# Performance work log

Measured on AMD Instinct MI355X. Metric: run time of the kernel, lower is better.

The kernel has to match this reference:

```python
import jax, jax.numpy as jnp
import numpy as np

B, T, D, H = 8, 2048, 1024, 64

def setup_inputs() -> dict:
    key = jax.random.key(0)
    ks = jax.random.split(key, 4)
    s = 1.0 / np.sqrt(D)
    return {
        "x": jax.random.normal(ks[0], (B, T, D), dtype=jnp.float32),
        "Wk": jax.random.normal(ks[1], (D, H), dtype=jnp.float32) * s,
        "bk": jnp.zeros((H,), dtype=jnp.float32),
        "Wq": jax.random.normal(ks[2], (D, H), dtype=jnp.float32) * s,
        "bq": jnp.zeros((H,), dtype=jnp.float32),
        "Wv": jax.random.normal(ks[3], (D, H), dtype=jnp.float32) * s,
        "bv": jnp.zeros((H,), dtype=jnp.float32),
    }

def reference(x, Wk, bk, Wq, bq, Wv, bv):
    # Linear projections: [B, T, H]
    k = x @ Wk + bk
    q = x @ Wq + bq
    v = x @ Wv + bv
    hs = k.shape[-1]
    # Scaled scores [B, T, T]
    scores = jnp.einsum('bqh,bkh->bqk', q, k) * (1.0 / np.sqrt(hs))
    # Causal mask (tril): positions j > i get -inf
    t = x.shape[1]
    causal = jnp.tril(jnp.ones((t, t), dtype=bool))
    scores = jnp.where(causal, scores, -jnp.inf)
    attn = jax.nn.softmax(scores, axis=-1)
    # Dropout is identity in eval mode
    return jnp.einsum('bqk,bkh->bqh', attn, v)
```

## Files before the change

kernel.cpp:

```cpp
#include <hip/hip_runtime.h>
#include <hip/hip_bf16.h>
#include <cmath>

#define B_ 8
#define T_ 2048
#define D_ 1024
#define H_ 64

typedef __bf16 bf16x8 __attribute__((ext_vector_type(8)));
typedef __bf16 bf16x4 __attribute__((ext_vector_type(4)));
typedef float f32x4 __attribute__((ext_vector_type(4)));

#define QSCALE 0.18033688011112042f

__device__ __forceinline__ void async_copy16(const void* g, void* lds) {
  __builtin_amdgcn_global_load_lds(
      (const __attribute__((address_space(1))) unsigned int*)g,
      (__attribute__((address_space(3))) unsigned int*)lds,
      16, 0, 0);
}

__global__ __launch_bounds__(256)
void castw_kernel(const float* __restrict__ w0,
                  const float* __restrict__ w1,
                  const float* __restrict__ w2,
                  __bf16* __restrict__ Wt) {
  __shared__ float tile[64][65];
  const int mat = blockIdx.y;
  const float* w = (mat == 0) ? w0 : (mat == 1) ? w1 : w2;
  const int d0 = blockIdx.x * 64;
  const int t = threadIdx.x;
#pragma unroll
  for (int i = 0; i < 16; i++) {
    int idx = i * 256 + t;
    int dl = idx >> 6, h = idx & 63;
    tile[dl][h] = w[(size_t)(d0 + dl) * 64 + h];
  }
  __syncthreads();
  const int h = t >> 2;
  const int dc = (t & 3) * 16;
  bf16x8 o0, o1;
#pragma unroll
  for (int j = 0; j < 8; j++) {
    o0[j] = (__bf16)tile[dc + j][h];
    o1[j] = (__bf16)tile[dc + 8 + j][h];
  }
  bf16x8* dst = (bf16x8*)(Wt + (size_t)mat * 65536 + (size_t)h * 1024 + d0 + dc);
  dst[0] = o0;
  dst[1] = o1;
}

__global__ __launch_bounds__(256)
void proj_kernel(const float* __restrict__ x,
                 const __bf16* __restrict__ Wt,
                 const float* __restrict__ bq,
                 const float* __restrict__ bk,
                 const float* __restrict__ bv,
                 __bf16* __restrict__ qb,
                 __bf16* __restrict__ kb,
                 __bf16* __restrict__ vt) {
  __shared__ __align__(16) __bf16 xs[32 * 128];
  __shared__ __align__(16) __bf16 wsl[192 * 128];

  const int tid  = threadIdx.x;
  const int wv   = tid >> 6;
  const int lane = tid & 63;
  const int ln   = lane & 15;
  const int quad = lane >> 4;
  const int m0   = blockIdx.x * 32;

  f32x4 acc[6] = {};

  for (int s = 0; s < 8; s++) {
    const int k0 = s * 128;
    __syncthreads();

#pragma unroll
    for (int j = 0; j < 12; j++) {
      int i = wv * 12 + j;
      int grow = i * 4 + (lane >> 4);
      int kc = (lane & 15) ^ (grow & 15);
      const __bf16* gp = Wt + (size_t)grow * 1024 + k0 + kc * 8;
      async_copy16(gp, wsl + i * 512);
    }

#pragma unroll
    for (int u = 0; u < 2; u++)
#pragma unroll
      for (int kh = 0; kh < 2; kh++) {
        int row = (tid >> 4) + u * 16;
        int fi = (tid & 15) + kh * 16;
        float4 f = *(const float4*)(x + (size_t)(m0 + row) * D_ + k0 + fi * 4);
        bf16x4 hv;
        hv[0] = (__bf16)f.x; hv[1] = (__bf16)f.y;
        hv[2] = (__bf16)f.z; hv[3] = (__bf16)f.w;
        int ch = fi >> 1, half = fi & 1;
        *(bf16x4*)(xs + row * 128 + ((ch ^ (row & 15)) * 8) + half * 4) = hv;
      }

    __syncthreads();

#pragma unroll
    for (int ks = 0; ks < 4; ks++) {
      bf16x8 af[2];
#pragma unroll
      for (int mt = 0; mt < 2; mt++) {
        int m = mt * 16 + ln;
        af[mt] = *(const bf16x8*)(xs + m * 128 + (((ks * 4 + quad) ^ (m & 15)) * 8));
      }
#pragma unroll
      for (int nt = 0; nt < 3; nt++) {
        int col = wv * 48 + nt * 16 + ln;
        bf16x8 bf = *(const bf16x8*)(wsl + col * 128 + (((ks * 4 + quad) ^ (col & 15)) * 8));
#pragma unroll
        for (int mt = 0; mt < 2; mt++)
          acc[mt * 3 + nt] =
              __builtin_amdgcn_mfma_f32_16x16x32_bf16(af[mt], bf, acc[mt * 3 + nt], 0, 0, 0);
      }
    }
  }

#pragma unroll
  for (int nt = 0; nt < 3; nt++) {
    int idx = wv * 48 + nt * 16;
    int mat = idx >> 6;
    int h = (idx & 63) + ln;
    float bcol = ((mat == 0) ? bq : (mat == 1) ? bk : bv)[h];
#pragma unroll
    for (int mt = 0; mt < 2; mt++) {
      f32x4 a = acc[mt * 3 + nt];
      int grow0 = m0 + mt * 16 + quad * 4;
      if (mat == 0) {
#pragma unroll
        for (int r = 0; r < 4; r++)
          qb[(size_t)(grow0 + r) * 64 + h] = (__bf16)((a[r] + bcol) * QSCALE);
      } else if (mat == 1) {
#pragma unroll
        for (int r = 0; r < 4; r++)
          kb[(size_t)(grow0 + r) * 64 + h] = (__bf16)(a[r] + bcol);
      } else {
        int bb = grow0 >> 11, t0 = grow0 & 2047;
        bf16x4 pv;
#pragma unroll
        for (int r = 0; r < 4; r++)
          pv[r] = (__bf16)(a[r] + bcol);
        *(bf16x4*)(vt + (size_t)(bb * 64 + h) * T_ + t0) = pv;
      }
    }
  }
}

__global__ __launch_bounds__(256)
void attn_kernel(const __bf16* __restrict__ qb,
                 const __bf16* __restrict__ kb,
                 const __bf16* __restrict__ vt,
                 float* __restrict__ out) {
  __shared__ __align__(16) __bf16 pA[2][4][16][72];
  __shared__ float ml_m[4][16];
  __shared__ float ml_l[4][16];
  __shared__ float olds[4][16][64];

  const int tid   = threadIdx.x;
  const int wv    = tid >> 6;
  const int lane  = tid & 63;
  const int ln    = lane & 15;
  const int quad  = lane >> 4;
  const int b     = blockIdx.y;

  const int p     = ((blockIdx.y >> 2) & 1) ? blockIdx.x : 63 - blockIdx.x;
  const int jqL   = p, jqH = 127 - p;
  const int qbL   = jqL * 16, qbH = jqH * 16;
  const int ntL   = (jqL >> 2) + 1;
  const int ntH   = (jqH >> 2) + 1;

  const __bf16* Q = qb + (size_t)b * T_ * 64;
  const __bf16* K = kb + (size_t)b * T_ * 64;
  const __bf16* V = vt + (size_t)b * 64 * T_;

  bf16x8 qaL0 = *(const bf16x8*)(Q + (qbL + ln) * 64 + quad * 8);
  bf16x8 qaL1 = *(const bf16x8*)(Q + (qbL + ln) * 64 + 32 + quad * 8);
  bf16x8 qaH0 = *(const bf16x8*)(Q + (qbH + ln) * 64 + quad * 8);
  bf16x8 qaH1 = *(const bf16x8*)(Q + (qbH + ln) * 64 + 32 + quad * 8);

  f32x4 accL[4] = {}, accH[4] = {};
  float mL = -INFINITY, lL = 0.f, mH = -INFINITY, lH = 0.f;

  bf16x8 kfa[4], kfb[4], vfa[4], vfb[4];
#pragma unroll
  for (int h = 0; h < 4; h++) {
    const __bf16* kr = K + (size_t)(wv * 64 + h * 16 + ln) * 64 + quad * 8;
    kfa[h] = *(const bf16x8*)kr;
    kfb[h] = *(const bf16x8*)(kr + 32);
  }

  int jt = wv;

  for (; jt < ntL; jt += 4) {
    const int kv0 = jt * 64;

    f32x4 sH[4] = {}, sL[4] = {};
#pragma unroll
    for (int h = 0; h < 4; h++) {
      sH[h] = __builtin_amdgcn_mfma_f32_16x16x32_bf16(kfa[h], qaH0, sH[h], 0, 0, 0);
      sH[h] = __builtin_amdgcn_mfma_f32_16x16x32_bf16(kfb[h], qaH1, sH[h], 0, 0, 0);
      sL[h] = __builtin_amdgcn_mfma_f32_16x16x32_bf16(kfa[h], qaL0, sL[h], 0, 0, 0);
      sL[h] = __builtin_amdgcn_mfma_f32_16x16x32_bf16(kfb[h], qaL1, sL[h], 0, 0, 0);
    }

    if (jt + 4 < ntH) {
#pragma unroll
      for (int h = 0; h < 4; h++) {
        const __bf16* kr = K + (size_t)(kv0 + 256 + h * 16 + ln) * 64 + quad * 8;
        kfa[h] = *(const bf16x8*)kr;
        kfb[h] = *(const bf16x8*)(kr + 32);
      }
    }
#pragma unroll
    for (int nt = 0; nt < 4; nt++) {
      const __bf16* vr = V + (size_t)(nt * 16 + ln) * T_ + kv0 + quad * 8;
      vfa[nt] = *(const bf16x8*)vr;
      vfb[nt] = *(const bf16x8*)(vr + 32);
    }

    if (jt == ntL - 1) {
      const int lim = qbL + ln - kv0 - quad * 4;
#pragma unroll
      for (int h = 0; h < 4; h++)
#pragma unroll
        for (int r = 0; r < 4; r++)
          if (h * 16 + r > lim) sL[h][r] = -INFINITY;
    }

    float mxH = sH[0][0], mxL = sL[0][0];
#pragma unroll
    for (int h = 0; h < 4; h++)
#pragma unroll
      for (int r = 0; r < 4; r++) {
        mxH = fmaxf(mxH, sH[h][r]);
        mxL = fmaxf(mxL, sL[h][r]);
      }
    mxH = fmaxf(mxH, __shfl_xor(mxH, 16));
    mxL = fmaxf(mxL, __shfl_xor(mxL, 16));
    mxH = fmaxf(mxH, __shfl_xor(mxH, 32));
    mxL = fmaxf(mxL, __shfl_xor(mxL, 32));

    float mnH = fmaxf(mH, mxH), mnL = fmaxf(mL, mxL);
    float alH = __builtin_amdgcn_exp2f(mH - mnH);
    float alL = __builtin_amdgcn_exp2f(mL - mnL);
    mH = mnH; mL = mnL;

    float pH[4][4], pL[4][4], smH = 0.f, smL = 0.f;
#pragma unroll
    for (int h = 0; h < 4; h++)
#pragma unroll
      for (int r = 0; r < 4; r++) {
        pH[h][r] = __builtin_amdgcn_exp2f(sH[h][r] - mnH);
        pL[h][r] = __builtin_amdgcn_exp2f(sL[h][r] - mnL);
        smH += pH[h][r];
        smL += pL[h][r];
      }
    smH += __shfl_xor(smH, 16);  smL += __shfl_xor(smL, 16);
    smH += __shfl_xor(smH, 32);  smL += __shfl_xor(smL, 32);
    lH = lH * alH + smH;
    lL = lL * alL + smL;

    float arH[4], arL[4];
#pragma unroll
    for (int r = 0; r < 4; r++) {
      arH[r] = __shfl(alH, quad * 4 + r);
      arL[r] = __shfl(alL, quad * 4 + r);
    }
#pragma unroll
    for (int nt = 0; nt < 4; nt++)
#pragma unroll
      for (int r = 0; r < 4; r++) {
        accH[nt][r] *= arH[r];
        accL[nt][r] *= arL[r];
      }

#pragma unroll
    for (int h = 0; h < 4; h++) {
      bf16x4 ph, pl;
#pragma unroll
      for (int r = 0; r < 4; r++) { ph[r] = (__bf16)pH[h][r]; pl[r] = (__bf16)pL[h][r]; }
      *(bf16x4*)(&pA[1][wv][ln][h * 16 + quad * 4]) = ph;
      *(bf16x4*)(&pA[0][wv][ln][h * 16 + quad * 4]) = pl;
    }
    bf16x8 paH0 = *(const bf16x8*)(&pA[1][wv][ln][quad * 8]);
    bf16x8 paH1 = *(const bf16x8*)(&pA[1][wv][ln][32 + quad * 8]);
    bf16x8 paL0 = *(const bf16x8*)(&pA[0][wv][ln][quad * 8]);
    bf16x8 paL1 = *(const bf16x8*)(&pA[0][wv][ln][32 + quad * 8]);
#pragma unroll
    for (int nt = 0; nt < 4; nt++) {
      accH[nt] = __builtin_amdgcn_mfma_f32_16x16x32_bf16(paH0, vfa[nt], accH[nt], 0, 0, 0);
      accH[nt] = __builtin_amdgcn_mfma_f32_16x16x32_bf16(paH1, vfb[nt], accH[nt], 0, 0, 0);
      accL[nt] = __builtin_amdgcn_mfma_f32_16x16x32_bf16(paL0, vfa[nt], accL[nt], 0, 0, 0);
      accL[nt] = __builtin_amdgcn_mfma_f32_16x16x32_bf16(paL1, vfb[nt], accL[nt], 0, 0, 0);
    }
  }

  for (; jt < ntH; jt += 4) {
    const int kv0 = jt * 64;

    f32x4 sH[4] = {};
#pragma unroll
    for (int h = 0; h < 4; h++) {
      sH[h] = __builtin_amdgcn_mfma_f32_16x16x32_bf16(kfa[h], qaH0, sH[h], 0, 0, 0);
      sH[h] = __builtin_amdgcn_mfma_f32_16x16x32_bf16(kfb[h], qaH1, sH[h], 0, 0, 0);
    }

    if (jt + 4 < ntH) {
#pragma unroll
      for (int h = 0; h < 4; h++) {
        const __bf16* kr = K + (size_t)(kv0 + 256 + h * 16 + ln) * 64 + quad * 8;
        kfa[h] = *(const bf16x8*)kr;
        kfb[h] = *(const bf16x8*)(kr + 32);
      }
    }
#pragma unroll
    for (int nt = 0; nt < 4; nt++) {
      const __bf16* vr = V + (size_t)(nt * 16 + ln) * T_ + kv0 + quad * 8;
      vfa[nt] = *(const bf16x8*)vr;
      vfb[nt] = *(const bf16x8*)(vr + 32);
    }

    if (jt == ntH - 1) {
      const int lim = qbH + ln - kv0 - quad * 4;
#pragma unroll
      for (int h = 0; h < 4; h++)
#pragma unroll
        for (int r = 0; r < 4; r++)
          if (h * 16 + r > lim) sH[h][r] = -INFINITY;
    }

    float mxH = sH[0][0];
#pragma unroll
    for (int h = 0; h < 4; h++)
#pragma unroll
      for (int r = 0; r < 4; r++) mxH = fmaxf(mxH, sH[h][r]);
    mxH = fmaxf(mxH, __shfl_xor(mxH, 16));
    mxH = fmaxf(mxH, __shfl_xor(mxH, 32));

    float mnH = fmaxf(mH, mxH);
    float alH = __builtin_amdgcn_exp2f(mH - mnH);
    mH = mnH;

    float pH[4][4], smH = 0.f;
#pragma unroll
    for (int h = 0; h < 4; h++)
#pragma unroll
      for (int r = 0; r < 4; r++) {
        pH[h][r] = __builtin_amdgcn_exp2f(sH[h][r] - mnH);
        smH += pH[h][r];
      }
    smH += __shfl_xor(smH, 16);
    smH += __shfl_xor(smH, 32);
    lH = lH * alH + smH;

    float arH[4];
#pragma unroll
    for (int r = 0; r < 4; r++) arH[r] = __shfl(alH, quad * 4 + r);
#pragma unroll
    for (int nt = 0; nt < 4; nt++)
#pragma unroll
      for (int r = 0; r < 4; r++) accH[nt][r] *= arH[r];

#pragma unroll
    for (int h = 0; h < 4; h++) {
      bf16x4 ph;
#pragma unroll
      for (int r = 0; r < 4; r++) ph[r] = (__bf16)pH[h][r];
      *(bf16x4*)(&pA[1][wv][ln][h * 16 + quad * 4]) = ph;
    }
    bf16x8 paH0 = *(const bf16x8*)(&pA[1][wv][ln][quad * 8]);
    bf16x8 paH1 = *(const bf16x8*)(&pA[1][wv][ln][32 + quad * 8]);
#pragma unroll
    for (int nt = 0; nt < 4; nt++) {
      accH[nt] = __builtin_amdgcn_mfma_f32_16x16x32_bf16(paH0, vfa[nt], accH[nt], 0, 0, 0);
      accH[nt] = __builtin_amdgcn_mfma_f32_16x16x32_bf16(paH1, vfb[nt], accH[nt], 0, 0, 0);
    }
  }

#pragma unroll
  for (int side = 0; side < 2; side++) {
    const float m_i = side == 0 ? mL : mH;
    const float l_i = side == 0 ? lL : lH;
    const f32x4* acc = side == 0 ? accL : accH;
    const int qbase  = side == 0 ? qbL : qbH;

    __syncthreads();
    if (quad == 0) {
      ml_m[wv][ln] = m_i;
      ml_l[wv][ln] = l_i;
    }
    __syncthreads();

#pragma unroll
    for (int r = 0; r < 4; r++) {
      int row = quad * 4 + r;
      float mstar = fmaxf(fmaxf(ml_m[0][row], ml_m[1][row]),
                          fmaxf(ml_m[2][row], ml_m[3][row]));
      float factor = __builtin_amdgcn_exp2f(ml_m[wv][row] - mstar);
#pragma unroll
      for (int nt = 0; nt < 4; nt++)
        olds[wv][row][nt * 16 + ln] = acc[nt][r] * factor;
    }
    __syncthreads();

    {
      int row = tid >> 4;
      int h0 = (tid & 15) * 4;
      float mstar = fmaxf(fmaxf(ml_m[0][row], ml_m[1][row]),
                          fmaxf(ml_m[2][row], ml_m[3][row]));
      float ltot = 0.f;
#pragma unroll
      for (int w = 0; w < 4; w++)
        ltot += ml_l[w][row] * __builtin_amdgcn_exp2f(ml_m[w][row] - mstar);
      float inv = 1.0f / ltot;
      float4 o = {0.f, 0.f, 0.f, 0.f};
#pragma unroll
      for (int w = 0; w < 4; w++) {
        float4 t = *(const float4*)(&olds[w][row][h0]);
        o.x += t.x; o.y += t.y; o.z += t.z; o.w += t.w;
      }
      o.x *= inv; o.y *= inv; o.z *= inv; o.w *= inv;
      *(float4*)(out + ((size_t)(b * T_ + qbase + row)) * 64 + h0) = o;
    }
  }
}

extern "C" void kernel_launch(void* const* d_in, const int* in_sizes, int n_in,
                              void* d_out, int out_size, void* d_ws, size_t ws_size,
                              hipStream_t stream) {
  const float* x  = (const float*)d_in[0];
  const float* Wk = (const float*)d_in[1];
  const float* bk = (const float*)d_in[2];
  const float* Wq = (const float*)d_in[3];
  const float* bq = (const float*)d_in[4];
  const float* Wv = (const float*)d_in[5];
  const float* bv = (const float*)d_in[6];
  float* out = (float*)d_out;

  char* ws = (char*)d_ws;
  __bf16* qb = (__bf16*)(ws);
  __bf16* kb = (__bf16*)(ws + (size_t)2 * 1024 * 1024);
  __bf16* vt = (__bf16*)(ws + (size_t)4 * 1024 * 1024);
  __bf16* Wt = (__bf16*)(ws + (size_t)6 * 1024 * 1024);

  castw_kernel<<<dim3(16, 3), 256, 0, stream>>>(Wq, Wk, Wv, Wt);
  proj_kernel<<<512, 256, 0, stream>>>(x, Wt, bq, bk, bv, qb, kb, vt);
  attn_kernel<<<dim3(64, 8), 256, 0, stream>>>(qb, kb, vt, out);
}
```

Before: 140.3 us.

## Defer softmax rescaling, unroll high-side KV loop by two, streamline epilogue

Adds lazy online-softmax rescaling: the accumulator and running sum are rescaled only when some row's new max exceeds the stored max by more than a threshold, so most iterations skip the exp and multiply work. The high-only KV loop now processes two 64-key tiles per iteration with a single max/sum reduction, interleaving K and V loads between the MFMAs. The low-side partials are stashed to LDS early and the epilogue is restructured to apply per-wave scale factors during the reduction, which removes some barriers. Launch bounds now request 2 blocks per CU, which may limit registers; skipping rescales lets exp arguments reach up to the threshold, relying on fp32/bf16 headroom.

After: 141.2 us. About the same (+0.7%).

```diff
diff --git a/kernel.cpp b/kernel.cpp
--- a/kernel.cpp
+++ b/kernel.cpp
@@ -12,6 +12,7 @@
 typedef float f32x4 __attribute__((ext_vector_type(4)));
 
 #define QSCALE 0.18033688011112042f
+#define DEFER_THR 10.0f
 
 __device__ __forceinline__ void async_copy16(const void* g, void* lds) {
   __builtin_amdgcn_global_load_lds(
@@ -150,7 +151,7 @@
   }
 }
 
-__global__ __launch_bounds__(256)
+__global__ __launch_bounds__(256, 2)
 void attn_kernel(const __bf16* __restrict__ qb,
                  const __bf16* __restrict__ kb,
                  const __bf16* __restrict__ vt,
@@ -244,45 +245,53 @@
     mxH = fmaxf(mxH, __shfl_xor(mxH, 32));
     mxL = fmaxf(mxL, __shfl_xor(mxL, 32));
 
-    float mnH = fmaxf(mH, mxH), mnL = fmaxf(mL, mxL);
-    float alH = __builtin_amdgcn_exp2f(mH - mnH);
-    float alL = __builtin_amdgcn_exp2f(mL - mnL);
-    mH = mnH; mL = mnL;
-
-    float pH[4][4], pL[4][4], smH = 0.f, smL = 0.f;
+    if (!__all(mxH <= mH + DEFER_THR)) {
+      float mn = fmaxf(mH, mxH);
+      float al = __builtin_amdgcn_exp2f(mH - mn);
+      mH = mn;
+      lH *= al;
+      float ar[4];
+#pragma unroll
+      for (int r = 0; r < 4; r++) ar[r] = __shfl(al, quad * 4 + r);
+#pragma unroll
+      for (int nt = 0; nt < 4; nt++)
+#pragma unroll
+        for (int r = 0; r < 4; r++) accH[nt][r] *= ar[r];
+    }
+    if (!__all(mxL <= mL + DEFER_THR)) {
+      float mn = fmaxf(mL, mxL);
+      float al = __builtin_amdgcn_exp2f(mL - mn);
+      mL = mn;
+      lL *= al;
+      float ar[4];
+#pragma unroll
+      for (int r = 0; r < 4; r++) ar[r] = __shfl(al, quad * 4 + r);
+#pragma unroll
+      for (int nt = 0; nt < 4; nt++)
+#pragma unroll
+        for (int r = 0; r < 4; r++) accL[nt][r] *= ar[r];
+    }
+
+    float pHv[4][4], pLv[4][4], smH = 0.f, smL = 0.f;
 #pragma unroll
     for (int h = 0; h < 4; h++)
 #pragma unroll
       for (int r = 0; r < 4; r++) {
-        pH[h][r] = __builtin_amdgcn_exp2f(sH[h][r] - mnH);
-        pL[h][r] = __builtin_amdgcn_exp2f(sL[h][r] - mnL);
-        smH += pH[h][r];
-        smL += pL[h][r];
+        pHv[h][r] = __builtin_amdgcn_exp2f(sH[h][r] - mH);
+        pLv[h][r] = __builtin_amdgcn_exp2f(sL[h][r] - mL);
+        smH += pHv[h][r];
+        smL += pLv[h][r];
       }
     smH += __shfl_xor(smH, 16);  smL += __shfl_xor(smL, 16);
     smH += __shfl_xor(smH, 32);  smL += __shfl_xor(smL, 32);
-    lH = lH * alH + smH;
-    lL = lL * alL + smL;
-
-    float arH[4], arL[4];
-#pragma unroll
-    for (int r = 0; r < 4; r++) {
-      arH[r] = __shfl(alH, quad * 4 + r);
-      arL[r] = __shfl(alL, quad * 4 + r);
-    }
-#pragma unroll
-    for (int nt = 0; nt < 4; nt++)
-#pragma unroll
-      for (int r = 0; r < 4; r++) {
-        accH[nt][r] *= arH[r];
-        accL[nt][r] *= arL[r];
-      }
+    lH += smH;
+    lL += smL;
 
 #pragma unroll
     for (int h = 0; h < 4; h++) {
       bf16x4 ph, pl;
 #pragma unroll
-      for (int r = 0; r < 4; r++) { ph[r] = (__bf16)pH[h][r]; pl[r] = (__bf16)pL[h][r]; }
+      for (int r = 0; r < 4; r++) { ph[r] = (__bf16)pHv[h][r]; pl[r] = (__bf16)pLv[h][r]; }
       *(bf16x4*)(&pA[1][wv][ln][h * 16 + quad * 4]) = ph;
       *(bf16x4*)(&pA[0][wv][ln][h * 16 + quad * 4]) = pl;
     }
@@ -299,23 +308,135 @@
     }
   }
 
-  for (; jt < ntH; jt += 4) {
-    const int kv0 = jt * 64;
-
-    f32x4 sH[4] = {};
-#pragma unroll
-    for (int h = 0; h < 4; h++) {
-      sH[h] = __builtin_amdgcn_mfma_f32_16x16x32_bf16(kfa[h], qaH0, sH[h], 0, 0, 0);
-      sH[h] = __builtin_amdgcn_mfma_f32_16x16x32_bf16(kfb[h], qaH1, sH[h], 0, 0, 0);
-    }
-
-    if (jt + 4 < ntH) {
+  if (quad == 0) { ml_m[wv][ln] = mL; ml_l[wv][ln] = lL; }
+#pragma unroll
+  for (int nt = 0; nt < 4; nt++)
+#pragma unroll
+    for (int r = 0; r < 4; r++)
+      olds[wv][quad * 4 + r][nt * 16 + ln] = accL[nt][r];
+
+  for (; jt + 4 < ntH; jt += 8) {
+    const int kv0a = jt * 64;
+    const int kv0b = kv0a + 256;
+
+    f32x4 sA[4] = {}, sB[4] = {};
+#pragma unroll
+    for (int h = 0; h < 4; h++) {
+      sA[h] = __builtin_amdgcn_mfma_f32_16x16x32_bf16(kfa[h], qaH0, sA[h], 0, 0, 0);
+      sA[h] = __builtin_amdgcn_mfma_f32_16x16x32_bf16(kfb[h], qaH1, sA[h], 0, 0, 0);
+    }
+#pragma unroll
+    for (int h = 0; h < 4; h++) {
+      const __bf16* kr = K + (size_t)(kv0b + h * 16 + ln) * 64 + quad * 8;
+      kfa[h] = *(const bf16x8*)kr;
+      kfb[h] = *(const bf16x8*)(kr + 32);
+    }
+#pragma unroll
+    for (int h = 0; h < 4; h++) {
+      sB[h] = __builtin_amdgcn_mfma_f32_16x16x32_bf16(kfa[h], qaH0, sB[h], 0, 0, 0);
+      sB[h] = __builtin_amdgcn_mfma_f32_16x16x32_bf16(kfb[h], qaH1, sB[h], 0, 0, 0);
+    }
+    if (jt + 8 < ntH) {
 #pragma unroll
       for (int h = 0; h < 4; h++) {
-        const __bf16* kr = K + (size_t)(kv0 + 256 + h * 16 + ln) * 64 + quad * 8;
+        const __bf16* kr = K + (size_t)(kv0a + 512 + h * 16 + ln) * 64 + quad * 8;
         kfa[h] = *(const bf16x8*)kr;
         kfb[h] = *(const bf16x8*)(kr + 32);
       }
+    }
+#pragma unroll
+    for (int nt = 0; nt < 4; nt++) {
+      const __bf16* vr = V + (size_t)(nt * 16 + ln) * T_ + kv0a + quad * 8;
+      vfa[nt] = *(const bf16x8*)vr;
+      vfb[nt] = *(const bf16x8*)(vr + 32);
+    }
+
+    if (jt + 4 == ntH - 1) {
+      const int lim = qbH + ln - kv0b - quad * 4;
+#pragma unroll
+      for (int h = 0; h < 4; h++)
+#pragma unroll
+        for (int r = 0; r < 4; r++)
+          if (h * 16 + r > lim) sB[h][r] = -INFINITY;
+    }
+
+    float mx = sA[0][0];
+#pragma unroll
+    for (int h = 0; h < 4; h++)
+#pragma unroll
+      for (int r = 0; r < 4; r++) {
+        mx = fmaxf(mx, sA[h][r]);
+        mx = fmaxf(mx, sB[h][r]);
+      }
+    mx = fmaxf(mx, __shfl_xor(mx, 16));
+    mx = fmaxf(mx, __shfl_xor(mx, 32));
+
+    if (!__all(mx <= mH + DEFER_THR)) {
+      float mn = fmaxf(mH, mx);
+      float al = __builtin_amdgcn_exp2f(mH - mn);
+      mH = mn;
+      lH *= al;
+      float ar[4];
+#pragma unroll
+      for (int r = 0; r < 4; r++) ar[r] = __shfl(al, quad * 4 + r);
+#pragma unroll
+      for (int nt = 0; nt < 4; nt++)
+#pragma unroll
+        for (int r = 0; r < 4; r++) accH[nt][r] *= ar[r];
+    }
+
+    float ppa[4][4], ppb[4][4], sm = 0.f;
+#pragma unroll
+    for (int h = 0; h < 4; h++)
+#pragma unroll
+      for (int r = 0; r < 4; r++) {
+        ppa[h][r] = __builtin_amdgcn_exp2f(sA[h][r] - mH);
+        ppb[h][r] = __builtin_amdgcn_exp2f(sB[h][r] - mH);
+        sm += ppa[h][r] + ppb[h][r];
+      }
+    sm += __shfl_xor(sm, 16);
+    sm += __shfl_xor(sm, 32);
+    lH += sm;
+
+#pragma unroll
+    for (int h = 0; h < 4; h++) {
+      bf16x4 pa4, pb4;
+#pragma unroll
+      for (int r = 0; r < 4; r++) { pa4[r] = (__bf16)ppa[h][r]; pb4[r] = (__bf16)ppb[h][r]; }
+      *(bf16x4*)(&pA[0][wv][ln][h * 16 + quad * 4]) = pa4;
+      *(bf16x4*)(&pA[1][wv][ln][h * 16 + quad * 4]) = pb4;
+    }
+    bf16x8 paA0 = *(const bf16x8*)(&pA[0][wv][ln][quad * 8]);
+    bf16x8 paA1 = *(const bf16x8*)(&pA[0][wv][ln][32 + quad * 8]);
+    bf16x8 paB0 = *(const bf16x8*)(&pA[1][wv][ln][quad * 8]);
+    bf16x8 paB1 = *(const bf16x8*)(&pA[1][wv][ln][32 + quad * 8]);
+
+#pragma unroll
+    for (int nt = 0; nt < 4; nt++) {
+      accH[nt] = __builtin_amdgcn_mfma_f32_16x16x32_bf16(paA0, vfa[nt], accH[nt], 0, 0, 0);
+      accH[nt] = __builtin_amdgcn_mfma_f32_16x16x32_bf16(paA1, vfb[nt], accH[nt], 0, 0, 0);
+    }
+#pragma unroll
+    for (int nt = 0; nt < 4; nt++) {
+      const __bf16* vr = V + (size_t)(nt * 16 + ln) * T_ + kv0b + quad * 8;
+      vfa[nt] = *(const bf16x8*)vr;
+      vfb[nt] = *(const bf16x8*)(vr + 32);
+    }
+#pragma unroll
+    for (int nt = 0; nt < 4; nt++) {
+      accH[nt] = __builtin_amdgcn_mfma_f32_16x16x32_bf16(paB0, vfa[nt], accH[nt], 0, 0, 0);
+      accH[nt] = __builtin_amdgcn_mfma_f32_16x16x32_bf16(paB1, vfb[nt], accH[nt], 0, 0, 0);
+    }
+  }
+
+  if (jt < ntH) {
+    const int kv0 = jt * 64;
+
+    f32x4 sT[4] = {};
+#pragma unroll
+    for (int h = 0; h < 4; h++) {
+      sT[h] = __builtin_amdgcn_mfma_f32_16x16x32_bf16(kfa[h], qaH0, sT[h], 0, 0, 0);
+      sT[h] = __builtin_amdgcn_mfma_f32_16x16x32_bf16(kfb[h], qaH1, sT[h], 0, 0, 0);
     }
 #pragma unroll
     for (int nt = 0; nt < 4; nt++) {
@@ -330,46 +451,48 @@
       for (int h = 0; h < 4; h++)
 #pragma unroll
         for (int r = 0; r < 4; r++)
-          if (h * 16 + r > lim) sH[h][r] = -INFINITY;
-    }
-
-    float mxH = sH[0][0];
+          if (h * 16 + r > lim) sT[h][r] = -INFINITY;
+    }
+
+    float mx = sT[0][0];
 #pragma unroll
     for (int h = 0; h < 4; h++)
 #pragma unroll
-      for (int r = 0; r < 4; r++) mxH = fmaxf(mxH, sH[h][r]);
-    mxH = fmaxf(mxH, __shfl_xor(mxH, 16));
-    mxH = fmaxf(mxH, __shfl_xor(mxH, 32));
-
-    float mnH = fmaxf(mH, mxH);
-    float alH = __builtin_amdgcn_exp2f(mH - mnH);
-    mH = mnH;
-
-    float pH[4][4], smH = 0.f;
+      for (int r = 0; r < 4; r++) mx = fmaxf(mx, sT[h][r]);
+    mx = fmaxf(mx, __shfl_xor(mx, 16));
+    mx = fmaxf(mx, __shfl_xor(mx, 32));
+
+    if (!__all(mx <= mH + DEFER_THR)) {
+      float mn = fmaxf(mH, mx);
+      float al = __builtin_amdgcn_exp2f(mH - mn);
+      mH = mn;
+      lH *= al;
+      float ar[4];
+#pragma unroll
+      for (int r = 0; r < 4; r++) ar[r] = __shfl(al, quad * 4 + r);
+#pragma unroll
+      for (int nt = 0; nt < 4; nt++)
+#pragma unroll
+        for (int r = 0; r < 4; r++) accH[nt][r] *= ar[r];
+    }
+
+    float pt[4][4], sm = 0.f;
 #pragma unroll
     for (int h = 0; h < 4; h++)
 #pragma unroll
       for (int r = 0; r < 4; r++) {
-        pH[h][r] = __builtin_amdgcn_exp2f(sH[h][r] - mnH);
-        smH += pH[h][r];
-      }
-    smH += __shfl_xor(smH, 16);
-    smH += __shfl_xor(smH, 32);
-    lH = lH * alH + smH;
-
-    float arH[4];
-#pragma unroll
-    for (int r = 0; r < 4; r++) arH[r] = __shfl(alH, quad * 4 + r);
-#pragma unroll
-    for (int nt = 0; nt < 4; nt++)
-#pragma unroll
-      for (int r = 0; r < 4; r++) accH[nt][r] *= arH[r];
+        pt[h][r] = __builtin_amdgcn_exp2f(sT[h][r] - mH);
+        sm += pt[h][r];
+      }
+    sm += __shfl_xor(sm, 16);
+    sm += __shfl_xor(sm, 32);
+    lH += sm;
 
 #pragma unroll
     for (int h = 0; h < 4; h++) {
       bf16x4 ph;
 #pragma unroll
-      for (int r = 0; r < 4; r++) ph[r] = (__bf16)pH[h][r];
+      for (int r = 0; r < 4; r++) ph[r] = (__bf16)pt[h][r];
       *(bf16x4*)(&pA[1][wv][ln][h * 16 + quad * 4]) = ph;
     }
     bf16x8 paH0 = *(const bf16x8*)(&pA[1][wv][ln][quad * 8]);
@@ -381,51 +504,60 @@
     }
   }
 
-#pragma unroll
-  for (int side = 0; side < 2; side++) {
-    const float m_i = side == 0 ? mL : mH;
-    const float l_i = side == 0 ? lL : lH;
-    const f32x4* acc = side == 0 ? accL : accH;
-    const int qbase  = side == 0 ? qbL : qbH;
-
-    __syncthreads();
-    if (quad == 0) {
-      ml_m[wv][ln] = m_i;
-      ml_l[wv][ln] = l_i;
-    }
-    __syncthreads();
-
-#pragma unroll
-    for (int r = 0; r < 4; r++) {
-      int row = quad * 4 + r;
-      float mstar = fmaxf(fmaxf(ml_m[0][row], ml_m[1][row]),
-                          fmaxf(ml_m[2][row], ml_m[3][row]));
-      float factor = __builtin_amdgcn_exp2f(ml_m[wv][row] - mstar);
-#pragma unroll
-      for (int nt = 0; nt < 4; nt++)
-        olds[wv][row][nt * 16 + ln] = acc[nt][r] * factor;
-    }
-    __syncthreads();
-
-    {
-      int row = tid >> 4;
-      int h0 = (tid & 15) * 4;
-      float mstar = fmaxf(fmaxf(ml_m[0][row], ml_m[1][row]),
-                          fmaxf(ml_m[2][row], ml_m[3][row]));
-      float ltot = 0.f;
-#pragma unroll
-      for (int w = 0; w < 4; w++)
-        ltot += ml_l[w][row] * __builtin_amdgcn_exp2f(ml_m[w][row] - mstar);
-      float inv = 1.0f / ltot;
-      float4 o = {0.f, 0.f, 0.f, 0.f};
-#pragma unroll
-      for (int w = 0; w < 4; w++) {
-        float4 t = *(const float4*)(&olds[w][row][h0]);
-        o.x += t.x; o.y += t.y; o.z += t.z; o.w += t.w;
-      }
-      o.x *= inv; o.y *= inv; o.z *= inv; o.w *= inv;
-      *(float4*)(out + ((size_t)(b * T_ + qbase + row)) * 64 + h0) = o;
-    }
+  __syncthreads();
+  {
+    const int row = tid >> 4;
+    const int h0 = (tid & 15) * 4;
+    float m0 = ml_m[0][row], m1 = ml_m[1][row], m2 = ml_m[2][row], m3 = ml_m[3][row];
+    float ms = fmaxf(fmaxf(m0, m1), fmaxf(m2, m3));
+    float f0 = __builtin_amdgcn_exp2f(m0 - ms);
+    float f1 = __builtin_amdgcn_exp2f(m1 - ms);
+    float f2 = __builtin_amdgcn_exp2f(m2 - ms);
+    float f3 = __builtin_amdgcn_exp2f(m3 - ms);
+    float ltot = ml_l[0][row] * f0 + ml_l[1][row] * f1 +
+                 ml_l[2][row] * f2 + ml_l[3][row] * f3;
+    float inv = 1.0f / ltot;
+    float4 t0 = *(const float4*)(&olds[0][row][h0]);
+    float4 t1 = *(const float4*)(&olds[1][row][h0]);
+    float4 t2 = *(const float4*)(&olds[2][row][h0]);
+    float4 t3 = *(const float4*)(&olds[3][row][h0]);
+    float4 o;
+    o.x = (t0.x * f0 + t1.x * f1 + t2.x * f2 + t3.x * f3) * inv;
+    o.y = (t0.y * f0 + t1.y * f1 + t2.y * f2 + t3.y * f3) * inv;
+    o.z = (t0.z * f0 + t1.z * f1 + t2.z * f2 + t3.z * f3) * inv;
+    o.w = (t0.w * f0 + t1.w * f1 + t2.w * f2 + t3.w * f3) * inv;
+    *(float4*)(out + ((size_t)(b * T_ + qbL + row)) * 64 + h0) = o;
+  }
+  __syncthreads();
+  if (quad == 0) { ml_m[wv][ln] = mH; ml_l[wv][ln] = lH; }
+#pragma unroll
+  for (int nt = 0; nt < 4; nt++)
+#pragma unroll
+    for (int r = 0; r < 4; r++)
+      olds[wv][quad * 4 + r][nt * 16 + ln] = accH[nt][r];
+  __syncthreads();
+  {
+    const int row = tid >> 4;
+    const int h0 = (tid & 15) * 4;
+    float m0 = ml_m[0][row], m1 = ml_m[1][row], m2 = ml_m[2][row], m3 = ml_m[3][row];
+    float ms = fmaxf(fmaxf(m0, m1), fmaxf(m2, m3));
+    float f0 = __builtin_amdgcn_exp2f(m0 - ms);
+    float f1 = __builtin_amdgcn_exp2f(m1 - ms);
+    float f2 = __builtin_amdgcn_exp2f(m2 - ms);
+    float f3 = __builtin_amdgcn_exp2f(m3 - ms);
+    float ltot = ml_l[0][row] * f0 + ml_l[1][row] * f1 +
+                 ml_l[2][row] * f2 + ml_l[3][row] * f3;
+    float inv = 1.0f / ltot;
+    float4 t0 = *(const float4*)(&olds[0][row][h0]);
+    float4 t1 = *(const float4*)(&olds[1][row][h0]);
+    float4 t2 = *(const float4*)(&olds[2][row][h0]);
+    float4 t3 = *(const float4*)(&olds[3][row][h0]);
+    float4 o;
+    o.x = (t0.x * f0 + t1.x * f1 + t2.x * f2 + t3.x * f3) * inv;
+    o.y = (t0.y * f0 + t1.y * f1 + t2.y * f2 + t3.y * f3) * inv;
+    o.z = (t0.z * f0 + t1.z * f1 + t2.z * f2 + t3.z * f3) * inv;
+    o.w = (t0.w * f0 + t1.w * f1 + t2.w * f2 + t3.w * f3) * inv;
+    *(float4*)(out + ((size_t)(b * T_ + qbH + row)) * 64 + h0) = o;
   }
 }
 
```
